# Kernel optimization log

Measured on AMD Instinct MI355X. Metric: run time of the kernel, lower is better.

The kernel has to match this reference:

```python
import jax, jax.numpy as jnp
import numpy as np

T, B, D, BF = 512, 256, 256, 2  # time (nodes/tree), batch, feature dim, branching factor


def setup_inputs() -> dict:
    key = jax.random.key(0)
    k1, k2, k3 = jax.random.split(key, 3)
    inputs = jax.random.normal(k1, (T, B, D), dtype=jnp.float32)
    # Valid postfix (shift-reduce) arity sequence: two leaves, then alternate
    # combine(2)/leaf(0) -> left-comb binary tree; keeps stack pointer in range.
    t = np.arange(T)
    ar = np.where((t >= 2) & (t % 2 == 0), 2, 0).astype(np.int64)
    arities = jnp.asarray(np.broadcast_to(ar[:, None], (T, B)))
    scale = 1.0 / np.sqrt(D)
    W_in = jax.random.normal(k2, (D, D), dtype=jnp.float32) * scale
    W_ch = jax.random.normal(k3, (BF, D, D), dtype=jnp.float32) * scale
    b = jnp.zeros((D,), dtype=jnp.float32)
    return {"inputs": inputs, "arities": arities, "W_in": W_in, "W_ch": W_ch, "b": b}


def reference(inputs, arities, W_in, W_ch, b):
    Tn, Bn, Dn = inputs.shape
    bf = W_ch.shape[0]
    k = jnp.arange(Bn)

    def unit(x, children):
        # tree-RNN cell: tanh(x@W_in + sum_i child_i@W_ch[i] + b)
        h = x @ W_in + b
        for i in range(bf):
            h = h + children[i] @ W_ch[i]
        return jnp.tanh(h)

    memory0 = jnp.zeros((Tn, Bn, Dn), dtype=inputs.dtype)
    stack0 = jnp.zeros((Bn, Tn + bf), dtype=arities.dtype)
    ptr0 = jnp.full((Bn,), bf - 1, dtype=arities.dtype)

    def step(carry, xs):
        memory, stack, ptr = carry
        x_t, ar, t = xs
        children = []
        for i in range(bf):
            idx = stack[k, ptr - i]                    # [B] top-of-stack pointers
            entry = memory[idx, k]                     # [B, D] gather child features
            mask = (ar > i).astype(entry.dtype)[:, None]
            children.append(entry * mask)              # zero absent children
        new_entry = unit(x_t, children)
        memory = memory.at[t].set(new_entry)           # scatter to memory slot t
        ptr = ptr - jnp.abs(ar) + 1                    # pop arity, push 1
        ignore = ar == -1
        # stack[k,ptr] *= ignore; += t*(1-ignore)  <=>  keep old if ignore else t
        stack = stack.at[k, ptr].set(jnp.where(ignore, stack[k, ptr], t))
        return (memory, stack, ptr), None

    (memory, stack, ptr), _ = jax.lax.scan(
        step, (memory0, stack0, ptr0), (inputs, arities, jnp.arange(Tn)))
    out = memory[stack[k, ptr], k]                     # [B, D] tree roots
    return (out, memory)
```

## Files before the change

kernel.cpp:

```cpp
#include <hip/hip_runtime.h>
#include <hip/hip_bf16.h>


constexpr int T = 512, B = 256, D = 256;

typedef float f2 __attribute__((ext_vector_type(2)));
typedef float f4 __attribute__((ext_vector_type(4)));

constexpr int WS_CNT  = 0;
constexpr int WS_ROOT = 16;
constexpr int WS_NW   = 272;
constexpr int WS_L0   = 1024;
constexpr int WS_L1   = WS_L0 + T * B;
constexpr int WS_WORK = WS_L1 + T * B;

__global__ __launch_bounds__(256) void k_stack(const int* __restrict__ ar,
                                               unsigned* __restrict__ ws) {
  __shared__ int ar_l[T];
  __shared__ int S[1024];
  __shared__ unsigned lbuf0[T];
  __shared__ unsigned lbuf1[T];
  __shared__ unsigned wbuf[1024];
  __shared__ int cnts[4];
  __shared__ unsigned base0, base1;

  int k = blockIdx.x;
  int tid = threadIdx.x;
  ar_l[tid]       = ar[tid * B + k];
  ar_l[tid + 256] = ar[(tid + 256) * B + k];
  S[tid] = 0; S[tid + 256] = 0; S[tid + 512] = 0; S[tid + 768] = 0;
  __syncthreads();

  if (tid == 0) {
    int ptr = 1;
    int top = 0, next = 0;
    int n0 = 0, n1 = 0, nw = 0;
    for (int t = 0; t < T; t++) {
      int a = ar_l[t];
      int aa = a < 0 ? -a : a;
      unsigned cc[2]; int ncc = 0;
      if (a > 0) {
        int c0 = top;
        if (ar_l[c0] <= 0)
          lbuf0[n0++] = (unsigned)c0 | ((unsigned)t << 9) | ((unsigned)k << 18);
        else
          cc[ncc++] = (unsigned)c0;
        if (a > 1) {
          int c1 = next;
          if (ar_l[c1] <= 0)
            lbuf1[n1++] = (unsigned)c1 | ((unsigned)t << 9) | ((unsigned)k << 18);
          else
            cc[ncc++] = (unsigned)c1 | (1u << 18);
        }
      }
      if (a >= 1) {
        if (ncc == 0) {
          wbuf[nw++] = (unsigned)t | (1u << 19) | (1u << 20);
        } else {
          for (int e = 0; e < ncc; e++) {
            unsigned w = (unsigned)t | ((cc[e] & 511u) << 9) |
                         (((cc[e] >> 18) & 1u) << 18) | (1u << 21);
            if (e == 0) w |= (1u << 19);
            if (e == ncc - 1) w |= (1u << 20);
            wbuf[nw++] = w;
          }
        }
      }
      int pnew = ptr - aa + 1;
      if (a != -1) {
        S[pnew & 1023] = t;
        if (aa == 0)      { next = top; top = t; }
        else if (aa == 1) { top = t; }
        else              { top = t; next = S[(pnew - 1) & 1023]; }
      }
      ptr = pnew;
    }
    cnts[0] = n0; cnts[1] = n1; cnts[2] = nw;
    cnts[3] = S[ptr & 1023];
    base0 = atomicAdd(ws + WS_CNT + 0, (unsigned)n0);
    base1 = atomicAdd(ws + WS_CNT + 1, (unsigned)n1);
  }
  __syncthreads();
  int n0 = cnts[0], n1 = cnts[1], nw = cnts[2];
  for (int i = tid; i < n0; i += 256) ws[WS_L0 + base0 + i] = lbuf0[i];
  for (int i = tid; i < n1; i += 256) ws[WS_L1 + base1 + i] = lbuf1[i];
  for (int i = tid; i < nw; i += 256) ws[WS_WORK + k * 1024 + i] = wbuf[i];
  if (tid == 0) { ws[WS_NW + k] = (unsigned)nw; ws[WS_ROOT + k] = (unsigned)cnts[3]; }
}

__global__ __launch_bounds__(256) void k_gemm_h(const float* __restrict__ X,
                                                const float* __restrict__ W,
                                                const float* __restrict__ bias,
                                                const int* __restrict__ ar,
                                                float* __restrict__ Hm) {
  int row0 = blockIdx.x * 64;
  __shared__ __align__(16) float As[16][68];
  __shared__ __align__(16) float Bs[16][256];
  __shared__ int lar[64];
  int tid = threadIdx.x;
  if (tid < 64) lar[tid] = ar[row0 + tid];
  int cq = tid & 31, rg = tid >> 5;
  float acc[8][8];
  float4 b_lo = *(const float4*)&bias[cq * 4];
  float4 b_hi = *(const float4*)&bias[128 + cq * 4];
#pragma unroll
  for (int rr = 0; rr < 8; rr++) {
    acc[rr][0] = b_lo.x; acc[rr][1] = b_lo.y; acc[rr][2] = b_lo.z; acc[rr][3] = b_lo.w;
    acc[rr][4] = b_hi.x; acc[rr][5] = b_hi.y; acc[rr][6] = b_hi.z; acc[rr][7] = b_hi.w;
  }
  int sr = tid >> 2;
  int skc = (tid & 3) * 4;
  for (int kk = 0; kk < 256; kk += 16) {
    float4 a4 = *(const float4*)&X[(row0 + sr) * 256 + kk + skc];
    As[skc + 0][sr] = a4.x; As[skc + 1][sr] = a4.y;
    As[skc + 2][sr] = a4.z; As[skc + 3][sr] = a4.w;
#pragma unroll
    for (int i = 0; i < 4; i++) {
      int idx = tid + i * 256;
      int r = idx >> 6, c4 = idx & 63;
      *(float4*)&Bs[r][c4 * 4] = *(const float4*)&W[(kk + r) * 256 + c4 * 4];
    }
    __syncthreads();
#pragma unroll
    for (int kc = 0; kc < 16; kc++) {
      float4 a0  = *(const float4*)&As[kc][rg * 8];
      float4 a1  = *(const float4*)&As[kc][rg * 8 + 4];
      float4 blo = *(const float4*)&Bs[kc][cq * 4];
      float4 bhi = *(const float4*)&Bs[kc][128 + cq * 4];
      float a[8]  = {a0.x, a0.y, a0.z, a0.w, a1.x, a1.y, a1.z, a1.w};
      float bb[8] = {blo.x, blo.y, blo.z, blo.w, bhi.x, bhi.y, bhi.z, bhi.w};
#pragma unroll
      for (int rr = 0; rr < 8; rr++)
#pragma unroll
        for (int q = 0; q < 8; q++) acc[rr][q] += a[rr] * bb[q];
    }
    __syncthreads();
  }
#pragma unroll
  for (int rr = 0; rr < 8; rr++) {
    int row = rg * 8 + rr;
    bool leaf = lar[row] <= 0;
    float4 lo, hi;
    lo.x = acc[rr][0]; lo.y = acc[rr][1]; lo.z = acc[rr][2]; lo.w = acc[rr][3];
    hi.x = acc[rr][4]; hi.y = acc[rr][5]; hi.z = acc[rr][6]; hi.w = acc[rr][7];
    if (leaf) {
      lo.x = tanhf(lo.x); lo.y = tanhf(lo.y); lo.z = tanhf(lo.z); lo.w = tanhf(lo.w);
      hi.x = tanhf(hi.x); hi.y = tanhf(hi.y); hi.z = tanhf(hi.z); hi.w = tanhf(hi.w);
    }
    float* dst = &Hm[(row0 + row) * 256];
    *(float4*)&dst[cq * 4] = lo;
    *(float4*)&dst[128 + cq * 4] = hi;
  }
}

__global__ __launch_bounds__(256) void k_leafgemm(const float* __restrict__ Hm,
                                                  float* __restrict__ Gm,
                                                  const float* __restrict__ Wch,
                                                  const unsigned* __restrict__ list,
                                                  const unsigned* __restrict__ cntp,
                                                  int which) {
  unsigned cnt = *cntp;
  unsigned tile0 = blockIdx.x * 64;
  if (tile0 >= cnt) return;
  int ne = (int)min(64u, cnt - tile0);
  __shared__ unsigned ent[64];
  __shared__ __align__(16) float As[16][68];
  __shared__ __align__(16) float Bs[16][256];
  int tid = threadIdx.x;
  if (tid < 64) ent[tid] = (tid < ne) ? list[tile0 + tid] : 0u;
  __syncthreads();
  const float* W = Wch + which * (D * D);
  int cq = tid & 31, rg = tid >> 5;
  float acc[8][8];
#pragma unroll
  for (int rr = 0; rr < 8; rr++)
#pragma unroll
    for (int q = 0; q < 8; q++) acc[rr][q] = 0.0f;
  int sr = tid >> 2;
  int skc = (tid & 3) * 4;
  unsigned se = ent[sr];
  int sc = (int)(se & 511u), skb = (int)((se >> 18) & 255u);
  const float* srow = &Hm[((sc << 8) + skb) * 256];
  for (int kk = 0; kk < 256; kk += 16) {
    float4 a4;
    if (sr < ne) a4 = *(const float4*)&srow[kk + skc];
    else { a4.x = a4.y = a4.z = a4.w = 0.0f; }
    As[skc + 0][sr] = a4.x; As[skc + 1][sr] = a4.y;
    As[skc + 2][sr] = a4.z; As[skc + 3][sr] = a4.w;
#pragma unroll
    for (int i = 0; i < 4; i++) {
      int idx = tid + i * 256;
      int r = idx >> 6, c4 = idx & 63;
      *(float4*)&Bs[r][c4 * 4] = *(const float4*)&W[(kk + r) * 256 + c4 * 4];
    }
    __syncthreads();
#pragma unroll
    for (int kc = 0; kc < 16; kc++) {
      float4 a0  = *(const float4*)&As[kc][rg * 8];
      float4 a1  = *(const float4*)&As[kc][rg * 8 + 4];
      float4 blo = *(const float4*)&Bs[kc][cq * 4];
      float4 bhi = *(const float4*)&Bs[kc][128 + cq * 4];
      float a[8]  = {a0.x, a0.y, a0.z, a0.w, a1.x, a1.y, a1.z, a1.w};
      float bb[8] = {blo.x, blo.y, blo.z, blo.w, bhi.x, bhi.y, bhi.z, bhi.w};
#pragma unroll
      for (int rr = 0; rr < 8; rr++)
#pragma unroll
        for (int q = 0; q < 8; q++) acc[rr][q] += a[rr] * bb[q];
    }
    __syncthreads();
  }
#pragma unroll
  for (int rr = 0; rr < 8; rr++) {
    int e = rg * 8 + rr;
    if (e < ne) {
      unsigned en = ent[e];
      int t = (int)((en >> 9) & 511u), kb = (int)((en >> 18) & 255u);
      float* dst = &Gm[((t << 8) + kb) * 256];
      float4 lo = *(const float4*)&dst[cq * 4];
      float4 hi = *(const float4*)&dst[128 + cq * 4];
      lo.x += acc[rr][0]; lo.y += acc[rr][1]; lo.z += acc[rr][2]; lo.w += acc[rr][3];
      hi.x += acc[rr][4]; hi.y += acc[rr][5]; hi.z += acc[rr][6]; hi.w += acc[rr][7];
      *(float4*)&dst[cq * 4] = lo;
      *(float4*)&dst[128 + cq * 4] = hi;
    }
  }
}

__global__ __launch_bounds__(512, 2) void k_seq(float* __restrict__ Mm,
                                                const float* __restrict__ Wch,
                                                const unsigned* __restrict__ ws) {
  int k = blockIdx.x;
  int tid = threadIdx.x;
  int cs = tid & 63;
  int ps = tid >> 6;
  __shared__ __align__(16) float crow[2][256];
  __shared__ __align__(16) float partial[8][256];
  f2 w01[32], w23[32];
  const float* W1 = Wch + D * D;
#pragma unroll
  for (int q = 0; q < 32; q++) {
    f4 wv = *(const f4*)&W1[(32 * ps + q) * 256 + 4 * cs];
    w01[q] = __builtin_shufflevector(wv, wv, 0, 1);
    w23[q] = __builtin_shufflevector(wv, wv, 2, 3);
  }
#pragma unroll
  for (int q = 0; q < 32; q++) {
    asm volatile("" : "+v"(w01[q]));
    asm volatile("" : "+v"(w23[q]));
  }
  int nw = (int)ws[WS_NW + k];
  const unsigned* work = ws + WS_WORK + k * 1024;
  int cached = -1;
  int rb = 0;
  __syncthreads();
  unsigned e = (nw > 0) ? work[0] : 0u;
  float nb = 0.0f;
  if (nw > 0 && ((e >> 19) & 1u) && tid < 256)
    nb = Mm[(((int)(e & 511u) << 8) + k) * 256 + tid];
  f2 a01 = {0.0f, 0.0f}, a23 = {0.0f, 0.0f};
  for (int n = 0; n < nw; n++) {
    unsigned cur = e;
    unsigned nxt = (n + 1 < nw) ? work[n + 1] : 0u;
    int t = (int)(cur & 511u), c = (int)((cur >> 9) & 511u);
    int wi = (int)((cur >> 18) & 1u);
    bool first = (cur >> 19) & 1u, last = (cur >> 20) & 1u, hasc = (cur >> 21) & 1u;
    if (first) { a01 = (f2){0.0f, 0.0f}; a23 = (f2){0.0f, 0.0f}; }
    float nb2 = 0.0f;
    if ((n + 1 < nw) && ((nxt >> 19) & 1u) && tid < 256)
      nb2 = Mm[(((int)(nxt & 511u) << 8) + k) * 256 + tid];
    if (hasc) {
      if (c != cached) {
        asm volatile("s_waitcnt vmcnt(0) lgkmcnt(0)" ::: "memory");
        __builtin_amdgcn_s_barrier();
        __builtin_amdgcn_sched_barrier(0);
        if (tid < 256) crow[rb][tid] = Mm[((c << 8) + k) * 256 + tid];
        cached = c;
        asm volatile("s_waitcnt vmcnt(0) lgkmcnt(0)" ::: "memory");
        __builtin_amdgcn_s_barrier();
        __builtin_amdgcn_sched_barrier(0);
      }
      const f4* hb = (const f4*)&crow[rb][32 * ps];
      if (wi == 1) {
#pragma unroll
        for (int q8 = 0; q8 < 8; q8++) {
          f4 h4 = hb[q8];
          f2 hx = {h4.x, h4.x}, hy = {h4.y, h4.y};
          f2 hz = {h4.z, h4.z}, hw = {h4.w, h4.w};
          a01 += hx * w01[4 * q8 + 0]; a23 += hx * w23[4 * q8 + 0];
          a01 += hy * w01[4 * q8 + 1]; a23 += hy * w23[4 * q8 + 1];
          a01 += hz * w01[4 * q8 + 2]; a23 += hz * w23[4 * q8 + 2];
          a01 += hw * w01[4 * q8 + 3]; a23 += hw * w23[4 * q8 + 3];
        }
      } else {
        const float* W0 = Wch;
#pragma unroll 4
        for (int q = 0; q < 32; q++) {
          float hv = crow[rb][32 * ps + q];
          f4 wv = *(const f4*)&W0[(32 * ps + q) * 256 + 4 * cs];
          a01.x += hv * wv.x; a01.y += hv * wv.y;
          a23.x += hv * wv.z; a23.y += hv * wv.w;
        }
      }
    }
    if (last) {
      f4 pv = {a01.x, a01.y, a23.x, a23.y};
      *(f4*)&partial[ps][4 * cs] = pv;
      __builtin_amdgcn_sched_barrier(0);
      asm volatile("s_waitcnt lgkmcnt(0)" ::: "memory");
      __builtin_amdgcn_s_barrier();
      __builtin_amdgcn_sched_barrier(0);
      if (tid < 256) {
        float s = nb;
#pragma unroll
        for (int m = 0; m < 8; m++) s += partial[m][tid];
        float v = tanhf(s);
        crow[rb ^ 1][tid] = v;
        Mm[((t << 8) + k) * 256 + tid] = v;
      }
      __builtin_amdgcn_sched_barrier(0);
      asm volatile("s_waitcnt lgkmcnt(0)" ::: "memory");
      __builtin_amdgcn_s_barrier();
      __builtin_amdgcn_sched_barrier(0);
      rb ^= 1;
      cached = t;
    }
    e = nxt; nb = nb2;
  }
}

__global__ __launch_bounds__(256) void k_root(const float* __restrict__ Mm,
                                              float* __restrict__ out,
                                              const unsigned* __restrict__ ws) {
  int k = blockIdx.x;
  unsigned r = ws[WS_ROOT + k];
  out[k * 256 + threadIdx.x] = Mm[(((int)r << 8) + k) * 256 + threadIdx.x];
}

extern "C" void kernel_launch(void* const* d_in, const int* in_sizes, int n_in,
                              void* d_out, int out_size, void* d_ws, size_t ws_size,
                              hipStream_t stream) {
  const float* X    = (const float*)d_in[0];
  const int*   AR   = (const int*)d_in[1];
  const float* Win  = (const float*)d_in[2];
  const float* Wch  = (const float*)d_in[3];
  const float* bias = (const float*)d_in[4];
  float* out = (float*)d_out;
  float* Mm  = out + B * D;
  unsigned* ws = (unsigned*)d_ws;

  hipMemsetAsync(d_ws, 0, 512, stream);
  k_stack<<<B, 256, 0, stream>>>(AR, ws);
  k_gemm_h<<<(T * B) / 64, 256, 0, stream>>>(X, Win, bias, AR, Mm);
  k_leafgemm<<<(T * B) / 64, 256, 0, stream>>>(Mm, Mm, Wch, ws + WS_L0, ws + WS_CNT + 0, 0);
  k_leafgemm<<<(T * B) / 64, 256, 0, stream>>>(Mm, Mm, Wch, ws + WS_L1, ws + WS_CNT + 1, 1);
  k_seq<<<B, 512, 0, stream>>>(Mm, Wch, ws);
  k_root<<<B, 256, 0, stream>>>(Mm, out, ws);
}
```

Measured before the change: 914.9 us.

## Enlarge GEMM tile, repartition sequential cell across 16 warps, fuse root gather

The input GEMM now computes a 128x256 tile per block, with each thread holding an 8x16 accumulator, which raises arithmetic intensity per shared-memory load. The sequential tree kernel splits the K dimension into 16 slices of 16 instead of 8 slices of 32, keeping 8 output columns per thread in registers. It also stages the work list into LDS and folds the root gather into its tail, removing one launch. The trade-offs are higher register pressure in both kernels and a 16-way partial reduction on every node.

```diff
diff --git a/kernel.cpp b/kernel.cpp
--- a/kernel.cpp
+++ b/kernel.cpp
@@ -93,46 +93,56 @@
                                                 const float* __restrict__ bias,
                                                 const int* __restrict__ ar,
                                                 float* __restrict__ Hm) {
-  int row0 = blockIdx.x * 64;
-  __shared__ __align__(16) float As[16][68];
+  int row0 = blockIdx.x * 128;
+  __shared__ __align__(16) float As[16][132];
   __shared__ __align__(16) float Bs[16][256];
-  __shared__ int lar[64];
+  __shared__ int lar[128];
   int tid = threadIdx.x;
-  if (tid < 64) lar[tid] = ar[row0 + tid];
-  int cq = tid & 31, rg = tid >> 5;
-  float acc[8][8];
-  float4 b_lo = *(const float4*)&bias[cq * 4];
-  float4 b_hi = *(const float4*)&bias[128 + cq * 4];
-#pragma unroll
-  for (int rr = 0; rr < 8; rr++) {
-    acc[rr][0] = b_lo.x; acc[rr][1] = b_lo.y; acc[rr][2] = b_lo.z; acc[rr][3] = b_lo.w;
-    acc[rr][4] = b_hi.x; acc[rr][5] = b_hi.y; acc[rr][6] = b_hi.z; acc[rr][7] = b_hi.w;
-  }
-  int sr = tid >> 2;
-  int skc = (tid & 3) * 4;
+  if (tid < 128) lar[tid] = ar[row0 + tid];
+  int cg = tid & 15;
+  int rg = tid >> 4;
+  float acc[8][16];
+  f4 bv[4];
+#pragma unroll
+  for (int qt = 0; qt < 4; qt++) bv[qt] = *(const f4*)&bias[64 * qt + cg * 4];
+#pragma unroll
+  for (int rr = 0; rr < 8; rr++)
+#pragma unroll
+    for (int qt = 0; qt < 4; qt++) {
+      acc[rr][4 * qt + 0] = bv[qt].x; acc[rr][4 * qt + 1] = bv[qt].y;
+      acc[rr][4 * qt + 2] = bv[qt].z; acc[rr][4 * qt + 3] = bv[qt].w;
+    }
+  int sr = tid >> 1;
+  int skc = (tid & 1) * 8;
   for (int kk = 0; kk < 256; kk += 16) {
-    float4 a4 = *(const float4*)&X[(row0 + sr) * 256 + kk + skc];
-    As[skc + 0][sr] = a4.x; As[skc + 1][sr] = a4.y;
-    As[skc + 2][sr] = a4.z; As[skc + 3][sr] = a4.w;
+    f4 xa = *(const f4*)&X[(row0 + sr) * 256 + kk + skc];
+    f4 xb = *(const f4*)&X[(row0 + sr) * 256 + kk + skc + 4];
+    As[skc + 0][sr] = xa.x; As[skc + 1][sr] = xa.y;
+    As[skc + 2][sr] = xa.z; As[skc + 3][sr] = xa.w;
+    As[skc + 4][sr] = xb.x; As[skc + 5][sr] = xb.y;
+    As[skc + 6][sr] = xb.z; As[skc + 7][sr] = xb.w;
 #pragma unroll
     for (int i = 0; i < 4; i++) {
       int idx = tid + i * 256;
       int r = idx >> 6, c4 = idx & 63;
-      *(float4*)&Bs[r][c4 * 4] = *(const float4*)&W[(kk + r) * 256 + c4 * 4];
+      *(f4*)&Bs[r][c4 * 4] = *(const f4*)&W[(kk + r) * 256 + c4 * 4];
     }
     __syncthreads();
 #pragma unroll
     for (int kc = 0; kc < 16; kc++) {
-      float4 a0  = *(const float4*)&As[kc][rg * 8];
-      float4 a1  = *(const float4*)&As[kc][rg * 8 + 4];
-      float4 blo = *(const float4*)&Bs[kc][cq * 4];
-      float4 bhi = *(const float4*)&Bs[kc][128 + cq * 4];
-      float a[8]  = {a0.x, a0.y, a0.z, a0.w, a1.x, a1.y, a1.z, a1.w};
-      float bb[8] = {blo.x, blo.y, blo.z, blo.w, bhi.x, bhi.y, bhi.z, bhi.w};
+      f4 A0 = *(const f4*)&As[kc][rg * 8];
+      f4 A1 = *(const f4*)&As[kc][rg * 8 + 4];
+      f4 B0 = *(const f4*)&Bs[kc][cg * 4];
+      f4 B1 = *(const f4*)&Bs[kc][64 + cg * 4];
+      f4 B2 = *(const f4*)&Bs[kc][128 + cg * 4];
+      f4 B3 = *(const f4*)&Bs[kc][192 + cg * 4];
+      float a[8]  = {A0.x, A0.y, A0.z, A0.w, A1.x, A1.y, A1.z, A1.w};
+      float b[16] = {B0.x, B0.y, B0.z, B0.w, B1.x, B1.y, B1.z, B1.w,
+                     B2.x, B2.y, B2.z, B2.w, B3.x, B3.y, B3.z, B3.w};
 #pragma unroll
       for (int rr = 0; rr < 8; rr++)
 #pragma unroll
-        for (int q = 0; q < 8; q++) acc[rr][q] += a[rr] * bb[q];
+        for (int q = 0; q < 16; q++) acc[rr][q] += a[rr] * b[q];
     }
     __syncthreads();
   }
@@ -140,16 +150,16 @@
   for (int rr = 0; rr < 8; rr++) {
     int row = rg * 8 + rr;
     bool leaf = lar[row] <= 0;
-    float4 lo, hi;
-    lo.x = acc[rr][0]; lo.y = acc[rr][1]; lo.z = acc[rr][2]; lo.w = acc[rr][3];
-    hi.x = acc[rr][4]; hi.y = acc[rr][5]; hi.z = acc[rr][6]; hi.w = acc[rr][7];
-    if (leaf) {
-      lo.x = tanhf(lo.x); lo.y = tanhf(lo.y); lo.z = tanhf(lo.z); lo.w = tanhf(lo.w);
-      hi.x = tanhf(hi.x); hi.y = tanhf(hi.y); hi.z = tanhf(hi.z); hi.w = tanhf(hi.w);
-    }
     float* dst = &Hm[(row0 + row) * 256];
-    *(float4*)&dst[cq * 4] = lo;
-    *(float4*)&dst[128 + cq * 4] = hi;
+#pragma unroll
+    for (int qt = 0; qt < 4; qt++) {
+      f4 v;
+      v.x = acc[rr][4 * qt + 0]; v.y = acc[rr][4 * qt + 1];
+      v.z = acc[rr][4 * qt + 2]; v.w = acc[rr][4 * qt + 3];
+      if (leaf) { v.x = tanhf(v.x); v.y = tanhf(v.y);
+                  v.z = tanhf(v.z); v.w = tanhf(v.w); }
+      *(f4*)&dst[64 * qt + cg * 4] = v;
+    }
   }
 }
 
@@ -227,44 +237,51 @@
 }
 
 __global__ __launch_bounds__(512, 2) void k_seq(float* __restrict__ Mm,
+                                                float* __restrict__ out,
                                                 const float* __restrict__ Wch,
                                                 const unsigned* __restrict__ ws) {
   int k = blockIdx.x;
   int tid = threadIdx.x;
-  int cs = tid & 63;
-  int ps = tid >> 6;
+  int cs = tid & 31;
+  int ps = tid >> 5;
   __shared__ __align__(16) float crow[2][256];
-  __shared__ __align__(16) float partial[8][256];
-  f2 w01[32], w23[32];
+  __shared__ __align__(16) float partial[16][260];
+  __shared__ unsigned wlds[1024];
+  f2 wa[64];
   const float* W1 = Wch + D * D;
 #pragma unroll
-  for (int q = 0; q < 32; q++) {
-    f4 wv = *(const f4*)&W1[(32 * ps + q) * 256 + 4 * cs];
-    w01[q] = __builtin_shufflevector(wv, wv, 0, 1);
-    w23[q] = __builtin_shufflevector(wv, wv, 2, 3);
-  }
-#pragma unroll
-  for (int q = 0; q < 32; q++) {
-    asm volatile("" : "+v"(w01[q]));
-    asm volatile("" : "+v"(w23[q]));
-  }
+  for (int p = 0; p < 16; p++) {
+    f4 w0 = *(const f4*)&W1[(16 * ps + p) * 256 + 8 * cs];
+    f4 w1 = *(const f4*)&W1[(16 * ps + p) * 256 + 8 * cs + 4];
+    wa[4 * p + 0] = __builtin_shufflevector(w0, w0, 0, 1);
+    wa[4 * p + 1] = __builtin_shufflevector(w0, w0, 2, 3);
+    wa[4 * p + 2] = __builtin_shufflevector(w1, w1, 0, 1);
+    wa[4 * p + 3] = __builtin_shufflevector(w1, w1, 2, 3);
+  }
+#pragma unroll
+  for (int q = 0; q < 64; q++) asm volatile("" : "+v"(wa[q]));
   int nw = (int)ws[WS_NW + k];
   const unsigned* work = ws + WS_WORK + k * 1024;
-  int cached = -1;
-  int rb = 0;
+  for (int i = tid; i < nw; i += 512) wlds[i] = work[i];
+  int cached = -1, rb = 0;
   __syncthreads();
-  unsigned e = (nw > 0) ? work[0] : 0u;
+  unsigned e = (nw > 0) ? wlds[0] : 0u;
   float nb = 0.0f;
   if (nw > 0 && ((e >> 19) & 1u) && tid < 256)
     nb = Mm[(((int)(e & 511u) << 8) + k) * 256 + tid];
-  f2 a01 = {0.0f, 0.0f}, a23 = {0.0f, 0.0f};
+  float gval = 0.0f;
+  f2 a0 = {0.f, 0.f}, a1 = {0.f, 0.f}, a2 = {0.f, 0.f}, a3 = {0.f, 0.f};
   for (int n = 0; n < nw; n++) {
     unsigned cur = e;
-    unsigned nxt = (n + 1 < nw) ? work[n + 1] : 0u;
+    unsigned nxt = (n + 1 < nw) ? wlds[n + 1] : 0u;
     int t = (int)(cur & 511u), c = (int)((cur >> 9) & 511u);
     int wi = (int)((cur >> 18) & 1u);
     bool first = (cur >> 19) & 1u, last = (cur >> 20) & 1u, hasc = (cur >> 21) & 1u;
-    if (first) { a01 = (f2){0.0f, 0.0f}; a23 = (f2){0.0f, 0.0f}; }
+    if (first) {
+      a0 = (f2){0.f, 0.f}; a1 = (f2){0.f, 0.f};
+      a2 = (f2){0.f, 0.f}; a3 = (f2){0.f, 0.f};
+      gval = nb;
+    }
     float nb2 = 0.0f;
     if ((n + 1 < nw) && ((nxt >> 19) & 1u) && tid < 256)
       nb2 = Mm[(((int)(nxt & 511u) << 8) + k) * 256 + tid];
@@ -279,40 +296,46 @@
         __builtin_amdgcn_s_barrier();
         __builtin_amdgcn_sched_barrier(0);
       }
-      const f4* hb = (const f4*)&crow[rb][32 * ps];
       if (wi == 1) {
-#pragma unroll
-        for (int q8 = 0; q8 < 8; q8++) {
-          f4 h4 = hb[q8];
-          f2 hx = {h4.x, h4.x}, hy = {h4.y, h4.y};
-          f2 hz = {h4.z, h4.z}, hw = {h4.w, h4.w};
-          a01 += hx * w01[4 * q8 + 0]; a23 += hx * w23[4 * q8 + 0];
-          a01 += hy * w01[4 * q8 + 1]; a23 += hy * w23[4 * q8 + 1];
-          a01 += hz * w01[4 * q8 + 2]; a23 += hz * w23[4 * q8 + 2];
-          a01 += hw * w01[4 * q8 + 3]; a23 += hw * w23[4 * q8 + 3];
+        const f4* hb = (const f4*)&crow[rb][16 * ps];
+        f4 h0 = hb[0], h1 = hb[1], h2 = hb[2], h3 = hb[3];
+        float hv[16];
+        hv[0] = h0.x; hv[1] = h0.y; hv[2]  = h0.z; hv[3]  = h0.w;
+        hv[4] = h1.x; hv[5] = h1.y; hv[6]  = h1.z; hv[7]  = h1.w;
+        hv[8] = h2.x; hv[9] = h2.y; hv[10] = h2.z; hv[11] = h2.w;
+        hv[12] = h3.x; hv[13] = h3.y; hv[14] = h3.z; hv[15] = h3.w;
+#pragma unroll
+        for (int p = 0; p < 16; p++) {
+          f2 hp = {hv[p], hv[p]};
+          a0 += hp * wa[4 * p + 0]; a1 += hp * wa[4 * p + 1];
+          a2 += hp * wa[4 * p + 2]; a3 += hp * wa[4 * p + 3];
         }
       } else {
         const float* W0 = Wch;
 #pragma unroll 4
-        for (int q = 0; q < 32; q++) {
-          float hv = crow[rb][32 * ps + q];
-          f4 wv = *(const f4*)&W0[(32 * ps + q) * 256 + 4 * cs];
-          a01.x += hv * wv.x; a01.y += hv * wv.y;
-          a23.x += hv * wv.z; a23.y += hv * wv.w;
+        for (int p = 0; p < 16; p++) {
+          float hvv = crow[rb][16 * ps + p];
+          f4 v0 = *(const f4*)&W0[(16 * ps + p) * 256 + 8 * cs];
+          f4 v1 = *(const f4*)&W0[(16 * ps + p) * 256 + 8 * cs + 4];
+          f2 hp = {hvv, hvv};
+          a0 += hp * (f2){v0.x, v0.y}; a1 += hp * (f2){v0.z, v0.w};
+          a2 += hp * (f2){v1.x, v1.y}; a3 += hp * (f2){v1.z, v1.w};
         }
       }
     }
     if (last) {
-      f4 pv = {a01.x, a01.y, a23.x, a23.y};
-      *(f4*)&partial[ps][4 * cs] = pv;
+      f4 p0 = {a0.x, a0.y, a1.x, a1.y};
+      f4 p1 = {a2.x, a2.y, a3.x, a3.y};
+      *(f4*)&partial[ps][8 * cs]     = p0;
+      *(f4*)&partial[ps][8 * cs + 4] = p1;
       __builtin_amdgcn_sched_barrier(0);
       asm volatile("s_waitcnt lgkmcnt(0)" ::: "memory");
       __builtin_amdgcn_s_barrier();
       __builtin_amdgcn_sched_barrier(0);
       if (tid < 256) {
-        float s = nb;
-#pragma unroll
-        for (int m = 0; m < 8; m++) s += partial[m][tid];
+        float s = gval;
+#pragma unroll
+        for (int m = 0; m < 16; m++) s += partial[m][tid];
         float v = tanhf(s);
         crow[rb ^ 1][tid] = v;
         Mm[((t << 8) + k) * 256 + tid] = v;
@@ -326,14 +349,11 @@
     }
     e = nxt; nb = nb2;
   }
-}
-
-__global__ __launch_bounds__(256) void k_root(const float* __restrict__ Mm,
-                                              float* __restrict__ out,
-                                              const unsigned* __restrict__ ws) {
-  int k = blockIdx.x;
+  asm volatile("s_waitcnt vmcnt(0) lgkmcnt(0)" ::: "memory");
+  __builtin_amdgcn_s_barrier();
   unsigned r = ws[WS_ROOT + k];
-  out[k * 256 + threadIdx.x] = Mm[(((int)r << 8) + k) * 256 + threadIdx.x];
+  if (tid < 256)
+    out[k * 256 + tid] = Mm[(((int)r << 8) + k) * 256 + tid];
 }
 
 extern "C" void kernel_launch(void* const* d_in, const int* in_sizes, int n_in,
@@ -350,9 +370,8 @@
 
   hipMemsetAsync(d_ws, 0, 512, stream);
   k_stack<<<B, 256, 0, stream>>>(AR, ws);
-  k_gemm_h<<<(T * B) / 64, 256, 0, stream>>>(X, Win, bias, AR, Mm);
+  k_gemm_h<<<(T * B) / 128, 256, 0, stream>>>(X, Win, bias, AR, Mm);
   k_leafgemm<<<(T * B) / 64, 256, 0, stream>>>(Mm, Mm, Wch, ws + WS_L0, ws + WS_CNT + 0, 0);
   k_leafgemm<<<(T * B) / 64, 256, 0, stream>>>(Mm, Mm, Wch, ws + WS_L1, ws + WS_CNT + 1, 1);
-  k_seq<<<B, 512, 0, stream>>>(Mm, Wch, ws);
-  k_root<<<B, 256, 0, stream>>>(Mm, out, ws);
-}
+  k_seq<<<B, 512, 0, stream>>>(Mm, out, Wch, ws);
+}
```

Result: slower. 973.5 us (+6.4%).
